# Kernel optimization log

Measured on AMD Instinct MI355X. Metric: run time of the kernel, lower is better.

Reference implementation:

```python
import jax, jax.numpy as jnp
import numpy as np

ENC_DIM = 1024
EMB_DIM = 256
K = 8192          # codebook size
COMMIT = 0.25
LN_EPS = 1e-5


def _ln(x, g, b):
    m = jnp.mean(x, axis=-1, keepdims=True)
    v = jnp.mean(jnp.square(x - m), axis=-1, keepdims=True)
    return (x - m) * jax.lax.rsqrt(v + LN_EPS) * g + b


def _mlp(x, W1, b1, g1, be1, W2, b2, g2, be2):
    # two feed_forward blocks: Linear -> ReLU -> LayerNorm
    x = _ln(jax.nn.relu(x @ W1 + b1), g1, be1)
    x = _ln(jax.nn.relu(x @ W2 + b2), g2, be2)
    return x


def setup_inputs() -> dict:
    key = jax.random.key(0)
    ks = jax.random.split(key, 10)
    d = ENC_DIM
    s = 1.0 / np.sqrt(d)
    inp = {"x": jax.random.normal(ks[0], (4, 2048, d), dtype=jnp.float32)}
    # encoder MLP (2 blocks)
    inp["We1"] = jax.random.uniform(ks[1], (d, d), jnp.float32, -s, s)
    inp["be1"] = jnp.zeros((d,), jnp.float32)
    inp["ge1"] = jnp.ones((d,), jnp.float32)
    inp["bne1"] = jnp.zeros((d,), jnp.float32)
    inp["We2"] = jax.random.uniform(ks[2], (d, d), jnp.float32, -s, s)
    inp["be2"] = jnp.zeros((d,), jnp.float32)
    inp["ge2"] = jnp.ones((d,), jnp.float32)
    inp["bne2"] = jnp.zeros((d,), jnp.float32)
    # decoder MLP (2 blocks)
    inp["Wd1"] = jax.random.uniform(ks[3], (d, d), jnp.float32, -s, s)
    inp["bd1"] = jnp.zeros((d,), jnp.float32)
    inp["gd1"] = jnp.ones((d,), jnp.float32)
    inp["bnd1"] = jnp.zeros((d,), jnp.float32)
    inp["Wd2"] = jax.random.uniform(ks[4], (d, d), jnp.float32, -s, s)
    inp["bd2"] = jnp.zeros((d,), jnp.float32)
    inp["gd2"] = jnp.ones((d,), jnp.float32)
    inp["bnd2"] = jnp.zeros((d,), jnp.float32)
    # codebook, init uniform(-1/K, 1/K)
    inp["codebook"] = jax.random.uniform(ks[5], (K, EMB_DIM), jnp.float32, -1.0 / K, 1.0 / K)
    return inp


def reference(x, We1, be1, ge1, bne1, We2, be2, ge2, bne2,
              Wd1, bd1, gd1, bnd1, Wd2, bd2, gd2, bnd2, codebook):
    bs, seq_len, d = x.shape
    z = _mlp(x, We1, be1, ge1, bne1, We2, be2, ge2, bne2)

    # ---- VectorQuantizer ----
    zg = z.reshape(bs, seq_len, -1, EMB_DIM)              # (b, s, g, e)
    flat = zg.reshape(-1, EMB_DIM)                        # (N, e)
    # pairwise squared distances to codebook: (N, K)
    dist = (jnp.sum(flat * flat, axis=1, keepdims=True)
            + jnp.sum(codebook * codebook, axis=1)
            - 2.0 * flat @ codebook.T)
    idx = jnp.argmin(dist, axis=1)                        # (N,)
    quantized = jnp.take(codebook, idx, axis=0).reshape(zg.shape)

    e_latent = jnp.mean(jnp.square(jax.lax.stop_gradient(quantized) - zg))
    q_latent = jnp.mean(jnp.square(quantized - jax.lax.stop_gradient(zg)))
    loss = q_latent + COMMIT * e_latent

    # straight-through estimator
    quantized = zg + jax.lax.stop_gradient(quantized - zg)
    quantized = quantized.reshape(bs, seq_len, d)

    # perplexity from code usage histogram
    n = flat.shape[0]
    counts = jnp.zeros((K,), x.dtype).at[idx].add(1.0)
    avg_probs = counts / n
    perplexity = jnp.exp(-jnp.sum(avg_probs * jnp.log(avg_probs + 1e-10)))

    out = _mlp(quantized, Wd1, bd1, gd1, bnd1, Wd2, bd2, gd2, bnd2)
    return (out, loss, perplexity)
```

## Files before the change

kernel.cpp:

```cpp
#include <hip/hip_runtime.h>
#include <stdint.h>


typedef short bf16x8 __attribute__((ext_vector_type(8)));
typedef float f32x4 __attribute__((ext_vector_type(4)));

__device__ __forceinline__ void gl2lds16(const void* g, void* l) {
  __builtin_amdgcn_global_load_lds(
      (const __attribute__((address_space(1))) void*)g,
      (__attribute__((address_space(3))) void*)l, 16, 0, 0);
}

__device__ __forceinline__ float bf2f(unsigned short u) {
  return __uint_as_float(((unsigned)u) << 16);
}
__device__ __forceinline__ unsigned short f2bf(float f) {
  unsigned x = __float_as_uint(f);
  unsigned r = (x + 0x7fffu + ((x >> 16) & 1u)) >> 16;
  return (unsigned short)r;
}
__device__ __forceinline__ unsigned long long packScore(float s, int code) {
  unsigned u = __float_as_uint(s);
  u = (u & 0x80000000u) ? ~u : (u | 0x80000000u);
  return ((unsigned long long)u << 32) | (unsigned)code;
}
__device__ __forceinline__ unsigned long long shflxor_u64(unsigned long long v, int m) {
  union { unsigned long long u; int i[2]; } a;
  a.u = v;
  a.i[0] = __shfl_xor(a.i[0], m);
  a.i[1] = __shfl_xor(a.i[1], m);
  return a.u;
}

__global__ __launch_bounds__(256)
void prep(const float* __restrict__ x, unsigned short* __restrict__ xb,
          const float* __restrict__ We1, const float* __restrict__ We2,
          const float* __restrict__ Wd1, const float* __restrict__ Wd2,
          unsigned short* __restrict__ wt0, unsigned short* __restrict__ wt1,
          unsigned short* __restrict__ wt2, unsigned short* __restrict__ wt3,
          const float* __restrict__ cb, unsigned short* __restrict__ cbb,
          float* __restrict__ cnorm, int* __restrict__ counts) {
  const int b = blockIdx.x;
  if (b < 2048) {
#pragma unroll
    for (int it = 0; it < 4; ++it) {
      int i = (it * 2048 + b) * 256 + threadIdx.x;
      float4 v = ((const float4*)x)[i];
      ((ushort4*)xb)[i] = make_ushort4(f2bf(v.x), f2bf(v.y), f2bf(v.z), f2bf(v.w));
    }
  } else if (b < 6144) {
    const int w = (b - 2048) >> 10;
    const int tile = (b - 2048) & 1023;
    const float* W = w == 0 ? We1 : w == 1 ? We2 : w == 2 ? Wd1 : Wd2;
    unsigned short* Wt = w == 0 ? wt0 : w == 1 ? wt1 : w == 2 ? wt2 : wt3;
    __shared__ float s[32][33];
    const int tx = threadIdx.x & 31, ty = threadIdx.x >> 5;
    const int bx = tile & 31, by = tile >> 5;
#pragma unroll
    for (int p = 0; p < 4; p++)
      s[ty + p * 8][tx] = W[(size_t)(by * 32 + ty + p * 8) * 1024 + bx * 32 + tx];
    __syncthreads();
#pragma unroll
    for (int p = 0; p < 4; p++)
      Wt[(size_t)(bx * 32 + ty + p * 8) * 1024 + by * 32 + tx] = f2bf(s[tx][ty + p * 8]);
  } else if (b < 6656) {
    const int bb = b - 6144;
#pragma unroll
    for (int it = 0; it < 4; ++it) {
      int i = (it * 512 + bb) * 256 + threadIdx.x;
      float4 v = ((const float4*)cb)[i];
      ((ushort4*)cbb)[i] = make_ushort4(f2bf(v.x), f2bf(v.y), f2bf(v.z), f2bf(v.w));
    }
  } else {
    const int row = (b - 6656) * 4 + (threadIdx.x >> 6);
    const int lane = threadIdx.x & 63;
    float4 v = ((const float4*)(cb + (size_t)row * 256))[lane];
    float s = v.x * v.x + v.y * v.y + v.z * v.z + v.w * v.w;
#pragma unroll
    for (int off = 32; off > 0; off >>= 1) s += __shfl_down(s, off);
    if (lane == 0) {
      cnorm[row] = s;
      counts[row] = 0;
    }
  }
}

__global__ __launch_bounds__(256, 2)
void gemm_bias_relu(const unsigned short* __restrict__ A, const unsigned short* __restrict__ Bt,
                    const float* __restrict__ bias, unsigned short* __restrict__ C,
                    int M, int N, int K) {
  __shared__ unsigned short As[2][128 * 64];
  __shared__ unsigned short Bs[2][128 * 64];
  const int t = threadIdx.x;
  const int wv = t >> 6, lane = t & 63;
  const int wm = wv >> 1, wn = wv & 1;
  const int quad = lane >> 4, l15 = lane & 15;

  const int lin = blockIdx.y * gridDim.x + blockIdx.x;
  const int cpx = (gridDim.x * gridDim.y) >> 3;
  const int nl = (lin & 7) * cpx + (lin >> 3);
  const int bx = nl % gridDim.x, by = nl / gridDim.x;
  const int row0 = by * 128, col0 = bx * 128;

  const int rsub = lane >> 3;
  const int dchunk = (lane & 7) ^ rsub;

  f32x4 acc[4][4];
#pragma unroll
  for (int i = 0; i < 4; i++)
#pragma unroll
    for (int j = 0; j < 4; j++) acc[i][j] = (f32x4){0.f, 0.f, 0.f, 0.f};

#pragma unroll
  for (int j = 0; j < 4; j++) {
    int slab = j * 4 + wv;
    int row = slab * 8 + rsub;
    gl2lds16(A + (size_t)(row0 + row) * K + dchunk * 8, &As[0][slab * 512]);
    gl2lds16(Bt + (size_t)(col0 + row) * K + dchunk * 8, &Bs[0][slab * 512]);
  }
  __syncthreads();

  int cur = 0;
  for (int k0 = 0; k0 < K; k0 += 64) {
    if (k0 + 64 < K) {
#pragma unroll
      for (int j = 0; j < 4; j++) {
        int slab = j * 4 + wv;
        int row = slab * 8 + rsub;
        gl2lds16(A + (size_t)(row0 + row) * K + (k0 + 64) + dchunk * 8,
                 &As[cur ^ 1][slab * 512]);
        gl2lds16(Bt + (size_t)(col0 + row) * K + (k0 + 64) + dchunk * 8,
                 &Bs[cur ^ 1][slab * 512]);
      }
    }
#pragma unroll
    for (int kk = 0; kk < 2; kk++) {
      bf16x8 af[4], bfr[4];
#pragma unroll
      for (int mt = 0; mt < 4; mt++) {
        int row = wm * 64 + mt * 16 + l15;
        af[mt] = *(const bf16x8*)(&As[cur][row * 64 + (((kk * 4 + quad) ^ (l15 & 7)) * 8)]);
      }
#pragma unroll
      for (int nt = 0; nt < 4; nt++) {
        int row = wn * 64 + nt * 16 + l15;
        bfr[nt] = *(const bf16x8*)(&Bs[cur][row * 64 + (((kk * 4 + quad) ^ (l15 & 7)) * 8)]);
      }
#pragma unroll
      for (int mt = 0; mt < 4; mt++)
#pragma unroll
        for (int nt = 0; nt < 4; nt++)
          acc[mt][nt] = __builtin_amdgcn_mfma_f32_16x16x32_bf16(af[mt], bfr[nt], acc[mt][nt], 0, 0, 0);
    }
    __syncthreads();
    cur ^= 1;
  }
#pragma unroll
  for (int mt = 0; mt < 4; mt++) {
#pragma unroll
    for (int nt = 0; nt < 4; nt++) {
      int col = col0 + wn * 64 + nt * 16 + l15;
      float b = bias[col];
#pragma unroll
      for (int r = 0; r < 4; r++) {
        int row = row0 + wm * 64 + mt * 16 + quad * 4 + r;
        float v = acc[mt][nt][r] + b;
        C[(size_t)row * N + col] = f2bf(v > 0.f ? v : 0.f);
      }
    }
  }
}

__global__ __launch_bounds__(256)
void ln_kernel(const unsigned short* __restrict__ X, const float* __restrict__ g,
               const float* __restrict__ b, unsigned short* __restrict__ obf,
               float* __restrict__ of32) {
  const int wave = threadIdx.x >> 6, lane = threadIdx.x & 63;
  const int row = blockIdx.x * 4 + wave;
  const unsigned short* xr = X + (size_t)row * 1024;
  bf16x8 u0 = *(const bf16x8*)(xr + lane * 8);
  bf16x8 u1 = *(const bf16x8*)(xr + 512 + lane * 8);
  float v0[8], v1[8];
  float s = 0.f, ss = 0.f;
#pragma unroll
  for (int i = 0; i < 8; i++) {
    v0[i] = bf2f((unsigned short)u0[i]);
    v1[i] = bf2f((unsigned short)u1[i]);
    s += v0[i] + v1[i];
    ss += v0[i] * v0[i] + v1[i] * v1[i];
  }
#pragma unroll
  for (int off = 32; off > 0; off >>= 1) {
    s += __shfl_down(s, off);
    ss += __shfl_down(ss, off);
  }
  s = __shfl(s, 0);
  ss = __shfl(ss, 0);
  const float m = s * (1.0f / 1024.0f);
  const float var = ss * (1.0f / 1024.0f) - m * m;
  const float rstd = 1.0f / sqrtf(var + 1e-5f);
  const int c0 = lane * 8;
  float4 ga = *(const float4*)(g + c0), gb4 = *(const float4*)(g + c0 + 4);
  float4 gc = *(const float4*)(g + 512 + c0), gd = *(const float4*)(g + 512 + c0 + 4);
  float4 ba = *(const float4*)(b + c0), bb4 = *(const float4*)(b + c0 + 4);
  float4 bc = *(const float4*)(b + 512 + c0), bd = *(const float4*)(b + 512 + c0 + 4);
  float o0[8], o1[8];
  const float* gl0 = &ga.x; const float* gl1 = &gc.x;
  float gv0[8] = {ga.x, ga.y, ga.z, ga.w, gb4.x, gb4.y, gb4.z, gb4.w};
  float gv1[8] = {gc.x, gc.y, gc.z, gc.w, gd.x, gd.y, gd.z, gd.w};
  float bv0[8] = {ba.x, ba.y, ba.z, ba.w, bb4.x, bb4.y, bb4.z, bb4.w};
  float bv1[8] = {bc.x, bc.y, bc.z, bc.w, bd.x, bd.y, bd.z, bd.w};
  (void)gl0; (void)gl1;
#pragma unroll
  for (int i = 0; i < 8; i++) {
    o0[i] = (v0[i] - m) * rstd * gv0[i] + bv0[i];
    o1[i] = (v1[i] - m) * rstd * gv1[i] + bv1[i];
  }
  if (obf) {
    bf16x8 q0, q1;
#pragma unroll
    for (int i = 0; i < 8; i++) { q0[i] = (short)f2bf(o0[i]); q1[i] = (short)f2bf(o1[i]); }
    *(bf16x8*)(obf + (size_t)row * 1024 + c0) = q0;
    *(bf16x8*)(obf + (size_t)row * 1024 + 512 + c0) = q1;
  } else {
    float* orow = of32 + (size_t)row * 1024;
    *(float4*)(orow + c0) = make_float4(o0[0], o0[1], o0[2], o0[3]);
    *(float4*)(orow + c0 + 4) = make_float4(o0[4], o0[5], o0[6], o0[7]);
    *(float4*)(orow + 512 + c0) = make_float4(o1[0], o1[1], o1[2], o1[3]);
    *(float4*)(orow + 512 + c0 + 4) = make_float4(o1[4], o1[5], o1[6], o1[7]);
  }
}

__global__ __launch_bounds__(256, 2)
void vq_dist(const unsigned short* __restrict__ Z, const unsigned short* __restrict__ Cb,
             const float* __restrict__ cnorm, const float* __restrict__ cbf,
             unsigned short* __restrict__ qb, int* __restrict__ counts,
             float* __restrict__ lpart) {
  __shared__ unsigned short Bs[2][64 * 256];
  __shared__ unsigned long long runmin[64];
  const int t = threadIdx.x;
  const int wv = t >> 6, lane = t & 63;
  const int quad = lane >> 4, l15 = lane & 15;
  const int row0 = blockIdx.x * 64;

  if (t < 64) runmin[t] = ~0ull;

  bf16x8 zf[4][8];
#pragma unroll
  for (int mt = 0; mt < 4; mt++)
#pragma unroll
    for (int ks = 0; ks < 8; ks++)
      zf[mt][ks] = *(const bf16x8*)(Z + (size_t)(row0 + mt * 16 + l15) * 256 + ks * 32 + quad * 8);

  float msc[4][4];
  int mcd[4][4];
#pragma unroll
  for (int mt = 0; mt < 4; mt++)
#pragma unroll
    for (int r = 0; r < 4; r++) { msc[mt][r] = 3.4e38f; mcd[mt][r] = 0; }

  const int dcode = lane >> 5;
  const int dgr = lane & 31;
  const int slot = wv * 16 + l15;
  const int rxor = l15 & 7;

  unsigned swz[8];
#pragma unroll
  for (int ks = 0; ks < 8; ks++)
    swz[ks] = (unsigned)slot * 256 + (unsigned)(((ks * 4 + quad) ^ rxor) * 8);

#pragma unroll
  for (int j = 0; j < 8; j++) {
    int slab = wv * 8 + j;
    int sl = slab * 2 + dcode;
    gl2lds16(Cb + (size_t)sl * 256 + ((dgr ^ (sl & 7)) * 8), &Bs[0][slab * 512]);
  }
  float cn_old = 3.4e38f;
  float cn_new = cnorm[slot];

  f32x4 pacc[4];
#pragma unroll
  for (int mt = 0; mt < 4; mt++) pacc[mt] = (f32x4){0.f, 0.f, 0.f, 0.f};

  for (int ch = 0; ch < 128; ch++) {
    const int cur = ch & 1;
    __builtin_amdgcn_s_waitcnt(0x3F70);

    {
      const int cb2 = ((ch + 1) & 127) * 64;
#pragma unroll
      for (int j = 0; j < 8; j++) {
        int slab = wv * 8 + j;
        int sl = slab * 2 + dcode;
        gl2lds16(Cb + (size_t)(cb2 + sl) * 256 + ((dgr ^ (sl & 7)) * 8),
                 &Bs[cur ^ 1][slab * 512]);
      }
    }

    const unsigned short* bsc = &Bs[cur][0];
    bf16x8 lbuf[8];
#pragma unroll
    for (int ks = 0; ks < 8; ks++)
      lbuf[ks] = *(const bf16x8*)(bsc + swz[ks]);

    {
      int code = (ch - 1) * 64 + slot;
#pragma unroll
      for (int mt = 0; mt < 4; mt++)
#pragma unroll
        for (int r = 0; r < 4; r++) {
          float sc = cn_old - 2.0f * pacc[mt][r];
          if (sc < msc[mt][r]) { msc[mt][r] = sc; mcd[mt][r] = code; }
        }
    }
    cn_old = cn_new;
    cn_new = cnorm[(((ch + 1) & 127) * 64) + slot];

#pragma unroll
    for (int ks = 0; ks < 8; ks++) {
      if (ks == 0) {
        const f32x4 z4 = (f32x4){0.f, 0.f, 0.f, 0.f};
#pragma unroll
        for (int mt = 0; mt < 4; mt++)
          pacc[mt] = __builtin_amdgcn_mfma_f32_16x16x32_bf16(zf[mt][0], lbuf[0], z4, 0, 0, 0);
      } else {
#pragma unroll
        for (int mt = 0; mt < 4; mt++)
          pacc[mt] = __builtin_amdgcn_mfma_f32_16x16x32_bf16(zf[mt][ks], lbuf[ks], pacc[mt], 0, 0, 0);
      }
    }
  }
  {
    int code = 127 * 64 + slot;
#pragma unroll
    for (int mt = 0; mt < 4; mt++)
#pragma unroll
      for (int r = 0; r < 4; r++) {
        float sc = cn_old - 2.0f * pacc[mt][r];
        if (sc < msc[mt][r]) { msc[mt][r] = sc; mcd[mt][r] = code; }
      }
  }

  __syncthreads();
#pragma unroll
  for (int mt = 0; mt < 4; mt++) {
#pragma unroll
    for (int r = 0; r < 4; r++) {
      unsigned long long bp = packScore(msc[mt][r], mcd[mt][r]);
#pragma unroll
      for (int m = 1; m < 16; m <<= 1) {
        unsigned long long o = shflxor_u64(bp, m);
        bp = o < bp ? o : bp;
      }
      if (l15 == 0) atomicMin(&runmin[mt * 16 + quad * 4 + r], bp);
    }
  }
  __syncthreads();

  float lp = 0.f;
#pragma unroll 4
  for (int rr = 0; rr < 16; rr++) {
    const int row = wv * 16 + rr;
    const int idx = (int)(runmin[row] & 0xFFFFFFFFull);
    float4 c = ((const float4*)(cbf + (size_t)idx * 256))[lane];
    ushort4 q = make_ushort4(f2bf(c.x), f2bf(c.y), f2bf(c.z), f2bf(c.w));
    ((ushort4*)(qb + (size_t)(row0 + row) * 256))[lane] = q;
    ushort4 z = ((const ushort4*)(Z + (size_t)(row0 + row) * 256))[lane];
    float dx = c.x - bf2f(z.x), dy = c.y - bf2f(z.y);
    float dz = c.z - bf2f(z.z), dw = c.w - bf2f(z.w);
    lp += dx * dx + dy * dy + dz * dz + dw * dw;
  }
  if (t < 64) atomicAdd(&counts[(int)(runmin[t] & 0xFFFFFFFFull)], 1);
#pragma unroll
  for (int off = 32; off > 0; off >>= 1) lp += __shfl_down(lp, off);
  __shared__ float sp[4];
  if (lane == 0) sp[wv] = lp;
  __syncthreads();
  if (t == 0) lpart[blockIdx.x] = sp[0] + sp[1] + sp[2] + sp[3];
}

__global__ __launch_bounds__(256)
void finalize(const int* __restrict__ counts, const float* __restrict__ lpart,
              float* __restrict__ out2) {
  const int t = threadIdx.x;
  double h = 0.0, l = 0.0;
  for (int i = t; i < 8192; i += 256) {
    double pr = (double)counts[i] * (1.0 / 32768.0);
    h += pr * log(pr + 1e-10);
  }
  for (int i = t; i < 512; i += 256) l += (double)lpart[i];
  __shared__ double sh[256], sl[256];
  sh[t] = h;
  sl[t] = l;
  __syncthreads();
  for (int w = 128; w > 0; w >>= 1) {
    if (t < w) { sh[t] += sh[t + w]; sl[t] += sl[t + w]; }
    __syncthreads();
  }
  if (t == 0) {
    out2[0] = (float)(1.25 * sl[0] * (1.0 / 8388608.0));
    out2[1] = (float)exp(-sh[0]);
  }
}

extern "C" void kernel_launch(void* const* d_in, const int* in_sizes, int n_in,
                              void* d_out, int out_size, void* d_ws, size_t ws_size,
                              hipStream_t stream) {
  const float* x = (const float*)d_in[0];
  const float* We1 = (const float*)d_in[1];
  const float* be1 = (const float*)d_in[2];
  const float* ge1 = (const float*)d_in[3];
  const float* bne1 = (const float*)d_in[4];
  const float* We2 = (const float*)d_in[5];
  const float* be2 = (const float*)d_in[6];
  const float* ge2 = (const float*)d_in[7];
  const float* bne2 = (const float*)d_in[8];
  const float* Wd1 = (const float*)d_in[9];
  const float* bd1 = (const float*)d_in[10];
  const float* gd1 = (const float*)d_in[11];
  const float* bnd1 = (const float*)d_in[12];
  const float* Wd2 = (const float*)d_in[13];
  const float* bd2 = (const float*)d_in[14];
  const float* gd2 = (const float*)d_in[15];
  const float* bnd2 = (const float*)d_in[16];
  const float* codebook = (const float*)d_in[17];
  float* out = (float*)d_out;

  char* w = (char*)d_ws;
  auto alloc = [&](size_t bytes) -> char* {
    char* p = w;
    w += (bytes + 255) & ~(size_t)255;
    return p;
  };
  unsigned short* xb = (unsigned short*)alloc((size_t)8192 * 1024 * 2);
  unsigned short* wt0 = (unsigned short*)alloc((size_t)1024 * 1024 * 2);
  unsigned short* wt1 = (unsigned short*)alloc((size_t)1024 * 1024 * 2);
  unsigned short* wt2 = (unsigned short*)alloc((size_t)1024 * 1024 * 2);
  unsigned short* wt3 = (unsigned short*)alloc((size_t)1024 * 1024 * 2);
  unsigned short* cbb = (unsigned short*)alloc((size_t)8192 * 256 * 2);
  float* cnorm = (float*)alloc((size_t)8192 * 4);
  unsigned short* act = (unsigned short*)alloc((size_t)8192 * 1024 * 2);
  unsigned short* yb = (unsigned short*)alloc((size_t)8192 * 1024 * 2);
  unsigned short* zb = (unsigned short*)alloc((size_t)8192 * 1024 * 2);
  unsigned short* qb = (unsigned short*)alloc((size_t)8192 * 1024 * 2);
  int* counts = (int*)alloc((size_t)8192 * 4);
  float* lpart = (float*)alloc((size_t)512 * 4);

  prep<<<8704, 256, 0, stream>>>(x, xb, We1, We2, Wd1, Wd2, wt0, wt1, wt2, wt3,
                                 codebook, cbb, cnorm, counts);

  dim3 gg(8, 64);
  gemm_bias_relu<<<gg, 256, 0, stream>>>(xb, wt0, be1, act, 8192, 1024, 1024);
  ln_kernel<<<2048, 256, 0, stream>>>(act, ge1, bne1, yb, nullptr);
  gemm_bias_relu<<<gg, 256, 0, stream>>>(yb, wt1, be2, act, 8192, 1024, 1024);
  ln_kernel<<<2048, 256, 0, stream>>>(act, ge2, bne2, zb, nullptr);
  vq_dist<<<512, 256, 0, stream>>>(zb, cbb, cnorm, codebook, qb, counts, lpart);
  gemm_bias_relu<<<gg, 256, 0, stream>>>(qb, wt2, bd1, act, 8192, 1024, 1024);
  ln_kernel<<<2048, 256, 0, stream>>>(act, gd1, bnd1, yb, nullptr);
  gemm_bias_relu<<<gg, 256, 0, stream>>>(yb, wt3, bd2, act, 8192, 1024, 1024);
  ln_kernel<<<2048, 256, 0, stream>>>(act, gd2, bnd2, nullptr, out);

  finalize<<<1, 256, 0, stream>>>(counts, lpart, out + 8388608);
}
```

Before: 428.2 us.

## Enlarge GEMM tile to 256x128 with 8 waves and split-phase prefetch

The bias+ReLU GEMM moves from 128x128 tiles with 4 waves to 256x128 tiles with 8 waves per block, and the grid is halved to match. Each B tile is now reused across twice as many rows, which cuts global traffic for B. The k-loop is split into two half-steps: the A prefetch is issued in the first half and the B prefetch in the second, with a barrier between them, so loads overlap with MFMA work. The larger LDS footprint (about 96KB per block) likely limits the kernel to one block per CU. The loop trip count is hardcoded for K=1024. A small unused-variable cleanup in the LayerNorm kernel is also included.

```diff
diff --git a/kernel.cpp b/kernel.cpp
--- a/kernel.cpp
+++ b/kernel.cpp
@@ -85,11 +85,11 @@
   }
 }
 
-__global__ __launch_bounds__(256, 2)
+__global__ __launch_bounds__(512, 2)
 void gemm_bias_relu(const unsigned short* __restrict__ A, const unsigned short* __restrict__ Bt,
                     const float* __restrict__ bias, unsigned short* __restrict__ C,
                     int M, int N, int K) {
-  __shared__ unsigned short As[2][128 * 64];
+  __shared__ unsigned short As[2][256 * 64];
   __shared__ unsigned short Bs[2][128 * 64];
   const int t = threadIdx.x;
   const int wv = t >> 6, lane = t & 63;
@@ -100,7 +100,7 @@
   const int cpx = (gridDim.x * gridDim.y) >> 3;
   const int nl = (lin & 7) * cpx + (lin >> 3);
   const int bx = nl % gridDim.x, by = nl / gridDim.x;
-  const int row0 = by * 128, col0 = bx * 128;
+  const int row0 = by * 256, col0 = bx * 128;
 
   const int rsub = lane >> 3;
   const int dchunk = (lane & 7) ^ rsub;
@@ -113,38 +113,42 @@
 
 #pragma unroll
   for (int j = 0; j < 4; j++) {
-    int slab = j * 4 + wv;
+    int slab = j * 8 + wv;
     int row = slab * 8 + rsub;
     gl2lds16(A + (size_t)(row0 + row) * K + dchunk * 8, &As[0][slab * 512]);
+  }
+#pragma unroll
+  for (int j = 0; j < 2; j++) {
+    int slab = j * 8 + wv;
+    int row = slab * 8 + rsub;
     gl2lds16(Bt + (size_t)(col0 + row) * K + dchunk * 8, &Bs[0][slab * 512]);
   }
-  __syncthreads();
-
-  int cur = 0;
-  for (int k0 = 0; k0 < K; k0 += 64) {
-    if (k0 + 64 < K) {
-#pragma unroll
-      for (int j = 0; j < 4; j++) {
-        int slab = j * 4 + wv;
-        int row = slab * 8 + rsub;
-        gl2lds16(A + (size_t)(row0 + row) * K + (k0 + 64) + dchunk * 8,
-                 &As[cur ^ 1][slab * 512]);
-        gl2lds16(Bt + (size_t)(col0 + row) * K + (k0 + 64) + dchunk * 8,
-                 &Bs[cur ^ 1][slab * 512]);
-      }
-    }
-#pragma unroll
-    for (int kk = 0; kk < 2; kk++) {
+
+  for (int T = 0; T < 16; T++) {
+    const int cur = T & 1;
+    const int kn = (T + 1) * 64;
+    __syncthreads();
+
+    {
       bf16x8 af[4], bfr[4];
 #pragma unroll
       for (int mt = 0; mt < 4; mt++) {
         int row = wm * 64 + mt * 16 + l15;
-        af[mt] = *(const bf16x8*)(&As[cur][row * 64 + (((kk * 4 + quad) ^ (l15 & 7)) * 8)]);
+        af[mt] = *(const bf16x8*)(&As[cur][row * 64 + ((quad ^ (l15 & 7)) * 8)]);
       }
 #pragma unroll
       for (int nt = 0; nt < 4; nt++) {
         int row = wn * 64 + nt * 16 + l15;
-        bfr[nt] = *(const bf16x8*)(&Bs[cur][row * 64 + (((kk * 4 + quad) ^ (l15 & 7)) * 8)]);
+        bfr[nt] = *(const bf16x8*)(&Bs[cur][row * 64 + ((quad ^ (l15 & 7)) * 8)]);
+      }
+      if (T + 1 < 16) {
+#pragma unroll
+        for (int j = 0; j < 4; j++) {
+          int slab = j * 8 + wv;
+          int row = slab * 8 + rsub;
+          gl2lds16(A + (size_t)(row0 + row) * K + kn + dchunk * 8,
+                   &As[cur ^ 1][slab * 512]);
+        }
       }
 #pragma unroll
       for (int mt = 0; mt < 4; mt++)
@@ -152,9 +156,37 @@
         for (int nt = 0; nt < 4; nt++)
           acc[mt][nt] = __builtin_amdgcn_mfma_f32_16x16x32_bf16(af[mt], bfr[nt], acc[mt][nt], 0, 0, 0);
     }
-    __syncthreads();
-    cur ^= 1;
-  }
+    __builtin_amdgcn_s_barrier();
+
+    {
+      bf16x8 af[4], bfr[4];
+#pragma unroll
+      for (int mt = 0; mt < 4; mt++) {
+        int row = wm * 64 + mt * 16 + l15;
+        af[mt] = *(const bf16x8*)(&As[cur][row * 64 + (((4 + quad) ^ (l15 & 7)) * 8)]);
+      }
+#pragma unroll
+      for (int nt = 0; nt < 4; nt++) {
+        int row = wn * 64 + nt * 16 + l15;
+        bfr[nt] = *(const bf16x8*)(&Bs[cur][row * 64 + (((4 + quad) ^ (l15 & 7)) * 8)]);
+      }
+      if (T + 1 < 16) {
+#pragma unroll
+        for (int j = 0; j < 2; j++) {
+          int slab = j * 8 + wv;
+          int row = slab * 8 + rsub;
+          gl2lds16(Bt + (size_t)(col0 + row) * K + kn + dchunk * 8,
+                   &Bs[cur ^ 1][slab * 512]);
+        }
+      }
+#pragma unroll
+      for (int mt = 0; mt < 4; mt++)
+#pragma unroll
+        for (int nt = 0; nt < 4; nt++)
+          acc[mt][nt] = __builtin_amdgcn_mfma_f32_16x16x32_bf16(af[mt], bfr[nt], acc[mt][nt], 0, 0, 0);
+    }
+  }
+
 #pragma unroll
   for (int mt = 0; mt < 4; mt++) {
 #pragma unroll
@@ -204,13 +236,11 @@
   float4 gc = *(const float4*)(g + 512 + c0), gd = *(const float4*)(g + 512 + c0 + 4);
   float4 ba = *(const float4*)(b + c0), bb4 = *(const float4*)(b + c0 + 4);
   float4 bc = *(const float4*)(b + 512 + c0), bd = *(const float4*)(b + 512 + c0 + 4);
-  float o0[8], o1[8];
-  const float* gl0 = &ga.x; const float* gl1 = &gc.x;
   float gv0[8] = {ga.x, ga.y, ga.z, ga.w, gb4.x, gb4.y, gb4.z, gb4.w};
   float gv1[8] = {gc.x, gc.y, gc.z, gc.w, gd.x, gd.y, gd.z, gd.w};
   float bv0[8] = {ba.x, ba.y, ba.z, ba.w, bb4.x, bb4.y, bb4.z, bb4.w};
   float bv1[8] = {bc.x, bc.y, bc.z, bc.w, bd.x, bd.y, bd.z, bd.w};
-  (void)gl0; (void)gl1;
+  float o0[8], o1[8];
 #pragma unroll
   for (int i = 0; i < 8; i++) {
     o0[i] = (v0[i] - m) * rstd * gv0[i] + bv0[i];
@@ -449,15 +479,15 @@
   prep<<<8704, 256, 0, stream>>>(x, xb, We1, We2, Wd1, Wd2, wt0, wt1, wt2, wt3,
                                  codebook, cbb, cnorm, counts);
 
-  dim3 gg(8, 64);
-  gemm_bias_relu<<<gg, 256, 0, stream>>>(xb, wt0, be1, act, 8192, 1024, 1024);
+  dim3 gg(8, 32);
+  gemm_bias_relu<<<gg, 512, 0, stream>>>(xb, wt0, be1, act, 8192, 1024, 1024);
   ln_kernel<<<2048, 256, 0, stream>>>(act, ge1, bne1, yb, nullptr);
-  gemm_bias_relu<<<gg, 256, 0, stream>>>(yb, wt1, be2, act, 8192, 1024, 1024);
+  gemm_bias_relu<<<gg, 512, 0, stream>>>(yb, wt1, be2, act, 8192, 1024, 1024);
   ln_kernel<<<2048, 256, 0, stream>>>(act, ge2, bne2, zb, nullptr);
   vq_dist<<<512, 256, 0, stream>>>(zb, cbb, cnorm, codebook, qb, counts, lpart);
-  gemm_bias_relu<<<gg, 256, 0, stream>>>(qb, wt2, bd1, act, 8192, 1024, 1024);
+  gemm_bias_relu<<<gg, 512, 0, stream>>>(qb, wt2, bd1, act, 8192, 1024, 1024);
   ln_kernel<<<2048, 256, 0, stream>>>(act, gd1, bnd1, yb, nullptr);
-  gemm_bias_relu<<<gg, 256, 0, stream>>>(yb, wt3, bd2, act, 8192, 1024, 1024);
+  gemm_bias_relu<<<gg, 512, 0, stream>>>(yb, wt3, bd2, act, 8192, 1024, 1024);
   ln_kernel<<<2048, 256, 0, stream>>>(act, gd2, bnd2, nullptr, out);
 
   finalize<<<1, 256, 0, stream>>>(counts, lpart, out + 8388608);
```

Result: slower. 440.0 us (+2.7%).

## Fold first LayerNorm of each MLP into the following GEMM via row stats

Applied to the files above, without the earlier changes.

The first GEMM of each MLP now accumulates per-row sum and sum-of-squares with atomics in its epilogue. The LN gamma is folded into the next layer's weights during prep, and the precomputed vectors u = gamma·W and v = beta·W let the next GEMM epilogue apply the normalization algebraically. This removes two standalone LayerNorm kernels and their activation round trips through memory. In exchange the epilogue gets more arithmetic and atomics, the GEMM consumes un-normalized bf16 activations (a precision change), and prep gets a slow serial column reduction over W.

```diff
diff --git a/kernel.cpp b/kernel.cpp
--- a/kernel.cpp
+++ b/kernel.cpp
@@ -39,7 +39,12 @@
           unsigned short* __restrict__ wt0, unsigned short* __restrict__ wt1,
           unsigned short* __restrict__ wt2, unsigned short* __restrict__ wt3,
           const float* __restrict__ cb, unsigned short* __restrict__ cbb,
-          float* __restrict__ cnorm, int* __restrict__ counts) {
+          float* __restrict__ cnorm, int* __restrict__ counts,
+          const float* __restrict__ ge1, const float* __restrict__ bne1,
+          const float* __restrict__ gd1, const float* __restrict__ bnd1,
+          float* __restrict__ u2, float* __restrict__ v2,
+          float* __restrict__ u4, float* __restrict__ v4,
+          float* __restrict__ stats1, float* __restrict__ stats3) {
   const int b = blockIdx.x;
   if (b < 2048) {
 #pragma unroll
@@ -53,6 +58,7 @@
     const int tile = (b - 2048) & 1023;
     const float* W = w == 0 ? We1 : w == 1 ? We2 : w == 2 ? Wd1 : Wd2;
     unsigned short* Wt = w == 0 ? wt0 : w == 1 ? wt1 : w == 2 ? wt2 : wt3;
+    const float* gs = w == 1 ? ge1 : (w == 3 ? gd1 : nullptr);
     __shared__ float s[32][33];
     const int tx = threadIdx.x & 31, ty = threadIdx.x >> 5;
     const int bx = tile & 31, by = tile >> 5;
@@ -60,9 +66,10 @@
     for (int p = 0; p < 4; p++)
       s[ty + p * 8][tx] = W[(size_t)(by * 32 + ty + p * 8) * 1024 + bx * 32 + tx];
     __syncthreads();
+    const float gk = gs ? gs[by * 32 + tx] : 1.0f;
 #pragma unroll
     for (int p = 0; p < 4; p++)
-      Wt[(size_t)(bx * 32 + ty + p * 8) * 1024 + by * 32 + tx] = f2bf(s[tx][ty + p * 8]);
+      Wt[(size_t)(bx * 32 + ty + p * 8) * 1024 + by * 32 + tx] = f2bf(s[tx][ty + p * 8] * gk);
   } else if (b < 6656) {
     const int bb = b - 6144;
 #pragma unroll
@@ -71,7 +78,7 @@
       float4 v = ((const float4*)cb)[i];
       ((ushort4*)cbb)[i] = make_ushort4(f2bf(v.x), f2bf(v.y), f2bf(v.z), f2bf(v.w));
     }
-  } else {
+  } else if (b < 8704) {
     const int row = (b - 6656) * 4 + (threadIdx.x >> 6);
     const int lane = threadIdx.x & 63;
     float4 v = ((const float4*)(cb + (size_t)row * 256))[lane];
@@ -82,12 +89,35 @@
       cnorm[row] = s;
       counts[row] = 0;
     }
+    if (lane < 2) {
+      stats1[2 * row + lane] = 0.f;
+      stats3[2 * row + lane] = 0.f;
+    }
+  } else {
+    const int idx = b - 8704;
+    const int msel = idx >> 2;
+    const int col = (idx & 3) * 256 + threadIdx.x;
+    const float* W = msel ? Wd2 : We2;
+    const float* g = msel ? gd1 : ge1;
+    const float* bn = msel ? bnd1 : bne1;
+    float* u = msel ? u4 : u2;
+    float* v = msel ? v4 : v2;
+    float us = 0.f, vs = 0.f;
+    for (int k = 0; k < 1024; k++) {
+      float w = W[(size_t)k * 1024 + col];
+      us += g[k] * w;
+      vs += bn[k] * w;
+    }
+    u[col] = us;
+    v[col] = vs;
   }
 }
 
 __global__ __launch_bounds__(256, 2)
 void gemm_bias_relu(const unsigned short* __restrict__ A, const unsigned short* __restrict__ Bt,
                     const float* __restrict__ bias, unsigned short* __restrict__ C,
+                    const float* __restrict__ statsIn, const float* __restrict__ uvec,
+                    const float* __restrict__ vvec, float* __restrict__ statsOut,
                     int M, int N, int K) {
   __shared__ unsigned short As[2][128 * 64];
   __shared__ unsigned short Bs[2][128 * 64];
@@ -155,19 +185,63 @@
     __syncthreads();
     cur ^= 1;
   }
+
+  float uc[4], vc[4], bc[4];
+#pragma unroll
+  for (int nt = 0; nt < 4; nt++) {
+    int col = col0 + wn * 64 + nt * 16 + l15;
+    bc[nt] = bias[col];
+    uc[nt] = statsIn ? uvec[col] : 0.f;
+    vc[nt] = statsIn ? vvec[col] : 0.f;
+  }
+  float psum[4][4], psq[4][4];
+#pragma unroll
+  for (int mt = 0; mt < 4; mt++)
+#pragma unroll
+    for (int r = 0; r < 4; r++) { psum[mt][r] = 0.f; psq[mt][r] = 0.f; }
+
 #pragma unroll
   for (int mt = 0; mt < 4; mt++) {
 #pragma unroll
-    for (int nt = 0; nt < 4; nt++) {
-      int col = col0 + wn * 64 + nt * 16 + l15;
-      float b = bias[col];
+    for (int r = 0; r < 4; r++) {
+      const int row = row0 + wm * 64 + mt * 16 + quad * 4 + r;
+      float scl = 1.f, sft = 0.f;
+      if (statsIn) {
+        float sm = statsIn[2 * row], sq = statsIn[2 * row + 1];
+        float mm = sm * (1.0f / 1024.0f);
+        float var = sq * (1.0f / 1024.0f) - mm * mm;
+        scl = rsqrtf(var + 1e-5f);
+        sft = scl * mm;
+      }
+#pragma unroll
+      for (int nt = 0; nt < 4; nt++) {
+        float v = acc[mt][nt][r];
+        v = statsIn ? (scl * v - sft * uc[nt] + vc[nt] + bc[nt]) : (v + bc[nt]);
+        v = v > 0.f ? v : 0.f;
+        int col = col0 + wn * 64 + nt * 16 + l15;
+        C[(size_t)row * N + col] = f2bf(v);
+        psum[mt][r] += v;
+        psq[mt][r] += v * v;
+      }
+    }
+  }
+  if (statsOut) {
+#pragma unroll
+    for (int mt = 0; mt < 4; mt++)
 #pragma unroll
       for (int r = 0; r < 4; r++) {
-        int row = row0 + wm * 64 + mt * 16 + quad * 4 + r;
-        float v = acc[mt][nt][r] + b;
-        C[(size_t)row * N + col] = f2bf(v > 0.f ? v : 0.f);
-      }
-    }
+        float s = psum[mt][r], q = psq[mt][r];
+#pragma unroll
+        for (int mk = 1; mk < 16; mk <<= 1) {
+          s += __shfl_xor(s, mk);
+          q += __shfl_xor(q, mk);
+        }
+        if (l15 == 0) {
+          const int row = row0 + wm * 64 + mt * 16 + quad * 4 + r;
+          atomicAdd(&statsOut[2 * row], s);
+          atomicAdd(&statsOut[2 * row + 1], q);
+        }
+      }
   }
 }
 
@@ -204,13 +278,11 @@
   float4 gc = *(const float4*)(g + 512 + c0), gd = *(const float4*)(g + 512 + c0 + 4);
   float4 ba = *(const float4*)(b + c0), bb4 = *(const float4*)(b + c0 + 4);
   float4 bc = *(const float4*)(b + 512 + c0), bd = *(const float4*)(b + 512 + c0 + 4);
-  float o0[8], o1[8];
-  const float* gl0 = &ga.x; const float* gl1 = &gc.x;
   float gv0[8] = {ga.x, ga.y, ga.z, ga.w, gb4.x, gb4.y, gb4.z, gb4.w};
   float gv1[8] = {gc.x, gc.y, gc.z, gc.w, gd.x, gd.y, gd.z, gd.w};
   float bv0[8] = {ba.x, ba.y, ba.z, ba.w, bb4.x, bb4.y, bb4.z, bb4.w};
   float bv1[8] = {bc.x, bc.y, bc.z, bc.w, bd.x, bd.y, bd.z, bd.w};
-  (void)gl0; (void)gl1;
+  float o0[8], o1[8];
 #pragma unroll
   for (int i = 0; i < 8; i++) {
     o0[i] = (v0[i] - m) * rstd * gv0[i] + bv0[i];
@@ -445,20 +517,30 @@
   unsigned short* qb = (unsigned short*)alloc((size_t)8192 * 1024 * 2);
   int* counts = (int*)alloc((size_t)8192 * 4);
   float* lpart = (float*)alloc((size_t)512 * 4);
-
-  prep<<<8704, 256, 0, stream>>>(x, xb, We1, We2, Wd1, Wd2, wt0, wt1, wt2, wt3,
-                                 codebook, cbb, cnorm, counts);
+  float* stats1 = (float*)alloc((size_t)8192 * 2 * 4);
+  float* stats3 = (float*)alloc((size_t)8192 * 2 * 4);
+  float* u2 = (float*)alloc((size_t)1024 * 4);
+  float* v2 = (float*)alloc((size_t)1024 * 4);
+  float* u4 = (float*)alloc((size_t)1024 * 4);
+  float* v4 = (float*)alloc((size_t)1024 * 4);
+
+  prep<<<8712, 256, 0, stream>>>(x, xb, We1, We2, Wd1, Wd2, wt0, wt1, wt2, wt3,
+                                 codebook, cbb, cnorm, counts,
+                                 ge1, bne1, gd1, bnd1, u2, v2, u4, v4,
+                                 stats1, stats3);
 
   dim3 gg(8, 64);
-  gemm_bias_relu<<<gg, 256, 0, stream>>>(xb, wt0, be1, act, 8192, 1024, 1024);
-  ln_kernel<<<2048, 256, 0, stream>>>(act, ge1, bne1, yb, nullptr);
-  gemm_bias_relu<<<gg, 256, 0, stream>>>(yb, wt1, be2, act, 8192, 1024, 1024);
-  ln_kernel<<<2048, 256, 0, stream>>>(act, ge2, bne2, zb, nullptr);
+  gemm_bias_relu<<<gg, 256, 0, stream>>>(xb, wt0, be1, act, nullptr, nullptr,
+                                         nullptr, stats1, 8192, 1024, 1024);
+  gemm_bias_relu<<<gg, 256, 0, stream>>>(act, wt1, be2, yb, stats1, u2, v2,
+                                         nullptr, 8192, 1024, 1024);
+  ln_kernel<<<2048, 256, 0, stream>>>(yb, ge2, bne2, zb, nullptr);
   vq_dist<<<512, 256, 0, stream>>>(zb, cbb, cnorm, codebook, qb, counts, lpart);
-  gemm_bias_relu<<<gg, 256, 0, stream>>>(qb, wt2, bd1, act, 8192, 1024, 1024);
-  ln_kernel<<<2048, 256, 0, stream>>>(act, gd1, bnd1, yb, nullptr);
-  gemm_bias_relu<<<gg, 256, 0, stream>>>(yb, wt3, bd2, act, 8192, 1024, 1024);
-  ln_kernel<<<2048, 256, 0, stream>>>(act, gd2, bnd2, nullptr, out);
+  gemm_bias_relu<<<gg, 256, 0, stream>>>(qb, wt2, bd1, act, nullptr, nullptr,
+                                         nullptr, stats3, 8192, 1024, 1024);
+  gemm_bias_relu<<<gg, 256, 0, stream>>>(act, wt3, bd2, yb, stats3, u4, v4,
+                                         nullptr, 8192, 1024, 1024);
+  ln_kernel<<<2048, 256, 0, stream>>>(yb, gd2, bnd2, nullptr, out);
 
   finalize<<<1, 256, 0, stream>>>(counts, lpart, out + 8388608);
 }
```

Result: slower. 478.9 us (+11.8%).

## Split VQ distance block into 8 waves sharing codebook tiles across row groups

Applied to the files above, without the earlier changes.

The vq_dist kernel moves from 4 waves to 8 waves per block. Each wave now covers 32 rows instead of 64, with two row groups sharing each LDS codebook chunk. Per-wave registers drop (zf, pacc and lbuf are halved), and LDS reads of the B fragments are software-pipelined inside the k loop. The per-chunk waitcnt becomes a full __syncthreads, which adds block-wide synchronisation in exchange for more waves available to hide latency.

```diff
diff --git a/kernel.cpp b/kernel.cpp
--- a/kernel.cpp
+++ b/kernel.cpp
@@ -204,13 +204,11 @@
   float4 gc = *(const float4*)(g + 512 + c0), gd = *(const float4*)(g + 512 + c0 + 4);
   float4 ba = *(const float4*)(b + c0), bb4 = *(const float4*)(b + c0 + 4);
   float4 bc = *(const float4*)(b + 512 + c0), bd = *(const float4*)(b + 512 + c0 + 4);
-  float o0[8], o1[8];
-  const float* gl0 = &ga.x; const float* gl1 = &gc.x;
   float gv0[8] = {ga.x, ga.y, ga.z, ga.w, gb4.x, gb4.y, gb4.z, gb4.w};
   float gv1[8] = {gc.x, gc.y, gc.z, gc.w, gd.x, gd.y, gd.z, gd.w};
   float bv0[8] = {ba.x, ba.y, ba.z, ba.w, bb4.x, bb4.y, bb4.z, bb4.w};
   float bv1[8] = {bc.x, bc.y, bc.z, bc.w, bd.x, bd.y, bd.z, bd.w};
-  (void)gl0; (void)gl1;
+  float o0[8], o1[8];
 #pragma unroll
   for (int i = 0; i < 8; i++) {
     o0[i] = (v0[i] - m) * rstd * gv0[i] + bv0[i];
@@ -231,7 +229,7 @@
   }
 }
 
-__global__ __launch_bounds__(256, 2)
+__global__ __launch_bounds__(512, 4)
 void vq_dist(const unsigned short* __restrict__ Z, const unsigned short* __restrict__ Cb,
              const float* __restrict__ cnorm, const float* __restrict__ cbf,
              unsigned short* __restrict__ qb, int* __restrict__ counts,
@@ -242,55 +240,54 @@
   const int wv = t >> 6, lane = t & 63;
   const int quad = lane >> 4, l15 = lane & 15;
   const int row0 = blockIdx.x * 64;
+  const int rg = wv >> 2;
+  const int cg = wv & 3;
 
   if (t < 64) runmin[t] = ~0ull;
 
-  bf16x8 zf[4][8];
-#pragma unroll
-  for (int mt = 0; mt < 4; mt++)
+  bf16x8 zf[2][8];
+#pragma unroll
+  for (int mt = 0; mt < 2; mt++)
 #pragma unroll
     for (int ks = 0; ks < 8; ks++)
-      zf[mt][ks] = *(const bf16x8*)(Z + (size_t)(row0 + mt * 16 + l15) * 256 + ks * 32 + quad * 8);
-
-  float msc[4][4];
-  int mcd[4][4];
-#pragma unroll
-  for (int mt = 0; mt < 4; mt++)
+      zf[mt][ks] = *(const bf16x8*)(Z + (size_t)(row0 + rg * 32 + mt * 16 + l15) * 256 +
+                                    ks * 32 + quad * 8);
+
+  float msc[2][4];
+  int mcd[2][4];
+#pragma unroll
+  for (int mt = 0; mt < 2; mt++)
 #pragma unroll
     for (int r = 0; r < 4; r++) { msc[mt][r] = 3.4e38f; mcd[mt][r] = 0; }
 
   const int dcode = lane >> 5;
   const int dgr = lane & 31;
-  const int slot = wv * 16 + l15;
+  const int slot = cg * 16 + l15;
   const int rxor = l15 & 7;
-
-  unsigned swz[8];
-#pragma unroll
-  for (int ks = 0; ks < 8; ks++)
-    swz[ks] = (unsigned)slot * 256 + (unsigned)(((ks * 4 + quad) ^ rxor) * 8);
-
-#pragma unroll
-  for (int j = 0; j < 8; j++) {
-    int slab = wv * 8 + j;
+  const unsigned sbase = (unsigned)slot * 256;
+
+#pragma unroll
+  for (int j = 0; j < 4; j++) {
+    int slab = wv * 4 + j;
     int sl = slab * 2 + dcode;
     gl2lds16(Cb + (size_t)sl * 256 + ((dgr ^ (sl & 7)) * 8), &Bs[0][slab * 512]);
   }
   float cn_old = 3.4e38f;
   float cn_new = cnorm[slot];
 
-  f32x4 pacc[4];
-#pragma unroll
-  for (int mt = 0; mt < 4; mt++) pacc[mt] = (f32x4){0.f, 0.f, 0.f, 0.f};
+  f32x4 pacc[2];
+#pragma unroll
+  for (int mt = 0; mt < 2; mt++) pacc[mt] = (f32x4){0.f, 0.f, 0.f, 0.f};
 
   for (int ch = 0; ch < 128; ch++) {
     const int cur = ch & 1;
-    __builtin_amdgcn_s_waitcnt(0x3F70);
+    __syncthreads();
 
     {
       const int cb2 = ((ch + 1) & 127) * 64;
 #pragma unroll
-      for (int j = 0; j < 8; j++) {
-        int slab = wv * 8 + j;
+      for (int j = 0; j < 4; j++) {
+        int slab = wv * 4 + j;
         int sl = slab * 2 + dcode;
         gl2lds16(Cb + (size_t)(cb2 + sl) * 256 + ((dgr ^ (sl & 7)) * 8),
                  &Bs[cur ^ 1][slab * 512]);
@@ -298,15 +295,15 @@
     }
 
     const unsigned short* bsc = &Bs[cur][0];
-    bf16x8 lbuf[8];
-#pragma unroll
-    for (int ks = 0; ks < 8; ks++)
-      lbuf[ks] = *(const bf16x8*)(bsc + swz[ks]);
+    bf16x8 lbuf[4];
+#pragma unroll
+    for (int ks = 0; ks < 4; ks++)
+      lbuf[ks] = *(const bf16x8*)(bsc + sbase + (((ks * 4 + quad) ^ rxor) * 8));
 
     {
       int code = (ch - 1) * 64 + slot;
 #pragma unroll
-      for (int mt = 0; mt < 4; mt++)
+      for (int mt = 0; mt < 2; mt++)
 #pragma unroll
         for (int r = 0; r < 4; r++) {
           float sc = cn_old - 2.0f * pacc[mt][r];
@@ -318,22 +315,24 @@
 
 #pragma unroll
     for (int ks = 0; ks < 8; ks++) {
+      bf16x8 lb = lbuf[ks & 3];
       if (ks == 0) {
         const f32x4 z4 = (f32x4){0.f, 0.f, 0.f, 0.f};
-#pragma unroll
-        for (int mt = 0; mt < 4; mt++)
-          pacc[mt] = __builtin_amdgcn_mfma_f32_16x16x32_bf16(zf[mt][0], lbuf[0], z4, 0, 0, 0);
+        pacc[0] = __builtin_amdgcn_mfma_f32_16x16x32_bf16(zf[0][0], lb, z4, 0, 0, 0);
+        pacc[1] = __builtin_amdgcn_mfma_f32_16x16x32_bf16(zf[1][0], lb, z4, 0, 0, 0);
       } else {
-#pragma unroll
-        for (int mt = 0; mt < 4; mt++)
-          pacc[mt] = __builtin_amdgcn_mfma_f32_16x16x32_bf16(zf[mt][ks], lbuf[ks], pacc[mt], 0, 0, 0);
-      }
+        pacc[0] = __builtin_amdgcn_mfma_f32_16x16x32_bf16(zf[0][ks], lb, pacc[0], 0, 0, 0);
+        pacc[1] = __builtin_amdgcn_mfma_f32_16x16x32_bf16(zf[1][ks], lb, pacc[1], 0, 0, 0);
+      }
+      if (ks < 4)
+        lbuf[ks & 3] =
+            *(const bf16x8*)(bsc + sbase + ((((ks + 4) * 4 + quad) ^ rxor) * 8));
     }
   }
   {
     int code = 127 * 64 + slot;
 #pragma unroll
-    for (int mt = 0; mt < 4; mt++)
+    for (int mt = 0; mt < 2; mt++)
 #pragma unroll
       for (int r = 0; r < 4; r++) {
         float sc = cn_old - 2.0f * pacc[mt][r];
@@ -343,7 +342,7 @@
 
   __syncthreads();
 #pragma unroll
-  for (int mt = 0; mt < 4; mt++) {
+  for (int mt = 0; mt < 2; mt++) {
 #pragma unroll
     for (int r = 0; r < 4; r++) {
       unsigned long long bp = packScore(msc[mt][r], mcd[mt][r]);
@@ -352,15 +351,16 @@
         unsigned long long o = shflxor_u64(bp, m);
         bp = o < bp ? o : bp;
       }
-      if (l15 == 0) atomicMin(&runmin[mt * 16 + quad * 4 + r], bp);
+      if (l15 == 0)
+        atomicMin(&runmin[rg * 32 + mt * 16 + quad * 4 + r], bp);
     }
   }
   __syncthreads();
 
   float lp = 0.f;
 #pragma unroll 4
-  for (int rr = 0; rr < 16; rr++) {
-    const int row = wv * 16 + rr;
+  for (int rr = 0; rr < 8; rr++) {
+    const int row = wv * 8 + rr;
     const int idx = (int)(runmin[row] & 0xFFFFFFFFull);
     float4 c = ((const float4*)(cbf + (size_t)idx * 256))[lane];
     ushort4 q = make_ushort4(f2bf(c.x), f2bf(c.y), f2bf(c.z), f2bf(c.w));
@@ -373,10 +373,11 @@
   if (t < 64) atomicAdd(&counts[(int)(runmin[t] & 0xFFFFFFFFull)], 1);
 #pragma unroll
   for (int off = 32; off > 0; off >>= 1) lp += __shfl_down(lp, off);
-  __shared__ float sp[4];
+  __shared__ float sp[8];
   if (lane == 0) sp[wv] = lp;
   __syncthreads();
-  if (t == 0) lpart[blockIdx.x] = sp[0] + sp[1] + sp[2] + sp[3];
+  if (t == 0)
+    lpart[blockIdx.x] = sp[0] + sp[1] + sp[2] + sp[3] + sp[4] + sp[5] + sp[6] + sp[7];
 }
 
 __global__ __launch_bounds__(256)
@@ -454,7 +455,7 @@
   ln_kernel<<<2048, 256, 0, stream>>>(act, ge1, bne1, yb, nullptr);
   gemm_bias_relu<<<gg, 256, 0, stream>>>(yb, wt1, be2, act, 8192, 1024, 1024);
   ln_kernel<<<2048, 256, 0, stream>>>(act, ge2, bne2, zb, nullptr);
-  vq_dist<<<512, 256, 0, stream>>>(zb, cbb, cnorm, codebook, qb, counts, lpart);
+  vq_dist<<<512, 512, 0, stream>>>(zb, cbb, cnorm, codebook, qb, counts, lpart);
   gemm_bias_relu<<<gg, 256, 0, stream>>>(qb, wt2, bd1, act, 8192, 1024, 1024);
   ln_kernel<<<2048, 256, 0, stream>>>(act, gd1, bnd1, yb, nullptr);
   gemm_bias_relu<<<gg, 256, 0, stream>>>(yb, wt3, bd2, act, 8192, 1024, 1024);
```

Result: slower. 502.8 us (+17.4%).
